# Kernel tuning notes

Hardware: AMD Instinct MI355X
Metric: run time of the kernel (lower is better)

The kernel has to match this reference:

```python
import jax, jax.numpy as jnp
import numpy as np


def force_fn(x):
    # Harmonic force F = -grad U, U(x) = 0.5 * ||x||^2 (Ornstein-Uhlenbeck).
    return -x


def setup_inputs() -> dict:
    key = jax.random.key(0)
    x0 = jax.random.normal(key, (100000, 3), dtype=jnp.float32)
    return {
        "x0": x0,
        "gamma": jnp.ones((1,), dtype=jnp.float32),
        "kT": jnp.ones((1,), dtype=jnp.float32),
        "dt": jnp.ones((1,), dtype=jnp.float32) * 0.01,
        "n_steps": 1000,
        "store_every": 10,
    }


def reference(x0, gamma, kT, dt, n_steps, store_every):
    # Overdamped Langevin: x_{t+1} = x_t + F(x_t)/gamma * dt + sqrt(2*kT*dt/gamma) * N(0, I)
    gamma_s = gamma.reshape(())
    kT_s = kT.reshape(())
    dt_s = dt.reshape(())
    noise_scale = jnp.sqrt(2.0 * kT_s * dt_s / gamma_s)

    n_chunks = n_steps // store_every  # trajectory stored every `store_every` steps
    keys = jax.random.split(jax.random.key(42), n_chunks * store_every)
    keys = keys.reshape((n_chunks, store_every))

    def step(x, k):
        noise = jax.random.normal(k, x.shape, x.dtype)
        x_new = x + force_fn(x) / gamma_s * dt_s + noise_scale * noise
        return x_new, None

    def chunk(x, ks):
        x, _ = jax.lax.scan(step, x, ks)
        return x, x  # carry and store the state after each chunk

    _, traj = jax.lax.scan(chunk, x0, keys)  # (n_chunks, N, 3)
    return jnp.concatenate([x0[None], traj], axis=0)  # (n_chunks + 1, N, 3)
```

## Files before the change

### kernel.cpp

```cpp
#include <hip/hip_runtime.h>


#define KCAP 1024

__device__ __forceinline__ unsigned rotl(unsigned v, int r) {
    return __builtin_rotateleft32(v, r);
}

__device__ __forceinline__ void tf2x32(unsigned k0, unsigned k1,
                                       unsigned x0, unsigned x1,
                                       unsigned &o0, unsigned &o1) {
    const unsigned ks2 = k0 ^ k1 ^ 0x1BD11BDAu;
    x0 += k0; x1 += k1;
#define RND(r) { x0 += x1; x1 = rotl(x1, r); x1 ^= x0; }
    RND(13) RND(15) RND(26) RND(6)
    x0 += k1;  x1 += ks2 + 1u;
    RND(17) RND(29) RND(16) RND(24)
    x0 += ks2; x1 += k0 + 2u;
    RND(13) RND(15) RND(26) RND(6)
    x0 += k0;  x1 += k1 + 3u;
    RND(17) RND(29) RND(16) RND(24)
    x0 += k1;  x1 += ks2 + 4u;
    RND(13) RND(15) RND(26) RND(6)
    x0 += ks2; x1 += k0 + 5u;
#undef RND
    o0 = x0; o1 = x1;
}

__device__ __forceinline__ float poly_lo(float w) {
    float p =        2.81022636e-08f;
    p = fmaf(p, w,   3.43273939e-07f);
    p = fmaf(p, w,  -3.5233877e-06f);
    p = fmaf(p, w,  -4.39150654e-06f);
    p = fmaf(p, w,   0.00021858087f);
    p = fmaf(p, w,  -0.00125372503f);
    p = fmaf(p, w,  -0.00417768164f);
    p = fmaf(p, w,   0.246640727f);
    p = fmaf(p, w,   1.50140941f);
    return p;
}
__device__ __forceinline__ float poly_hi(float s) {
    float p =       -0.000200214257f;
    p = fmaf(p, s,   0.000100950558f);
    p = fmaf(p, s,   0.00134934322f);
    p = fmaf(p, s,  -0.00367342844f);
    p = fmaf(p, s,   0.00573950773f);
    p = fmaf(p, s,  -0.0076224613f);
    p = fmaf(p, s,   0.00943887047f);
    p = fmaf(p, s,   1.00167406f);
    p = fmaf(p, s,   2.83297682f);
    return p;
}

__device__ __forceinline__ float lang_step(float x, uint4 k, unsigned t,
                                           float scale2, float na) {
    unsigned x1 = k.y + t;
    unsigned x0 = k.w + t;
    x1 = rotl(x1, 13) ^ x0;
#define RND(r) { x0 += x1; x1 = rotl(x1, r); x1 ^= x0; }
    RND(15) RND(26) RND(6)
    x0 += k.y; x1 += k.z + 1u;
    RND(17) RND(29) RND(16) RND(24)
    x0 += k.z; x1 += k.x + 2u;
    RND(13) RND(15) RND(26) RND(6)
    x0 += k.x; x1 += k.y + 3u;
    RND(17) RND(29) RND(16) RND(24)
    x0 += k.y; x1 += k.z + 4u;
    RND(13) RND(15) RND(26) RND(6)
    x0 += k.z; x1 += k.x + 5u;
#undef RND
    unsigned bits = x0 ^ x1;

    unsigned fb = (bits >> 9) | 0x3f800000u;
    float F = __uint_as_float(fb);
    float u = fmaf(F, 2.0f, -3.0f);
    u = fmaxf(u, -0.99999994f);
    float h = fmaf(-u, u, 1.0f);
#if __has_builtin(__builtin_amdgcn_logf)
    float l2 = __builtin_amdgcn_logf(h);
#else
    float l2 = __log2f(h);
#endif
    float p;
    if (__builtin_expect(__any(l2 <= -7.2134752f), 0)) {
        float w  = l2 * -0.69314718f;
        float p1 = poly_lo(w - 2.5f);
        float p2 = poly_hi(sqrtf(w) - 3.0f);
        p = (l2 > -7.2134752f) ? p1 : p2;
    } else {
        p = poly_lo(fmaf(l2, -0.69314718f, -2.5f));
    }
    return fmaf(scale2, p * u, fmaf(na, x, x));
}

__global__ __launch_bounds__(256) void expand_keys(uint4* __restrict__ kw) {
    unsigned j = blockIdx.x * 256 + threadIdx.x;
    if (j < KCAP) {
        unsigned b0, b1;
        tf2x32(0u, 42u, 0u, j, b0, b1);
        kw[j] = make_uint4(b0, b1, b0 ^ b1 ^ 0x1BD11BDAu, b0 + b1);
    }
}

template <bool GK>
__global__ __launch_bounds__(256) void OverdampedLangevin_62362925138458_kernel(
    const float* __restrict__ x0p,
    const float* __restrict__ gamma_p,
    const float* __restrict__ kT_p,
    const float* __restrict__ dt_p,
    const int*   __restrict__ nsteps_p,
    const int*   __restrict__ store_p,
    const uint4* __restrict__ kw,
    float*       __restrict__ out,
    int E)
{
    extern __shared__ uint4 ksh[];
    const int n_steps = *nsteps_p;
    const int store_every = *store_p;

    if (!GK) {
        const int nk = n_steps < KCAP ? n_steps : KCAP;
        for (int j = threadIdx.x; j < nk; j += blockDim.x) {
            unsigned b0, b1;
            tf2x32(0u, 42u, 0u, (unsigned)j, b0, b1);
            ksh[j] = make_uint4(b0, b1, b0 ^ b1 ^ 0x1BD11BDAu, b0 + b1);
        }
        __syncthreads();
    }

    const unsigned t = blockIdx.x * blockDim.x + threadIdx.x;
    if ((int)t >= E) return;

    const float g  = gamma_p[0];
    const float kT = kT_p[0];
    const float dt = dt_p[0];
    const float scale2 = sqrtf(2.0f * kT * dt / g) * 1.41421356f;
    const float na = -(dt / g);

    float x = x0p[t];
    out[t] = x;

    if (store_every == 10 && n_steps % 10 == 0 && n_steps <= KCAP) {
        const int nc = n_steps / 10;
        float* op = out + (size_t)E + t;
        int idx = 0;
        for (int c = 0; c < nc; ++c) {
#pragma unroll
            for (int s = 0; s < 10; ++s) {
                const uint4 k = GK ? kw[idx + s] : ksh[idx + s];
                x = lang_step(x, k, t, scale2, na);
            }
            idx += 10;
            *op = x;
            op += (size_t)E;
        }
    } else {
        int frame = 1, since = 0;
#pragma unroll 1
        for (int s = 0; s < n_steps; ++s) {
            uint4 k;
            if (s < KCAP) k = GK ? kw[s] : ksh[s];
            else {
                unsigned b0, b1;
                tf2x32(0u, 42u, 0u, (unsigned)s, b0, b1);
                k = make_uint4(b0, b1, b0 ^ b1 ^ 0x1BD11BDAu, b0 + b1);
            }
            x = lang_step(x, k, t, scale2, na);
            if (++since == store_every) {
                since = 0;
                out[(size_t)frame * (size_t)E + t] = x;
                ++frame;
            }
        }
    }
}

extern "C" void kernel_launch(void* const* d_in, const int* in_sizes, int n_in,
                              void* d_out, int out_size, void* d_ws, size_t ws_size,
                              hipStream_t stream) {
    const float* x0    = (const float*)d_in[0];
    const float* gam   = (const float*)d_in[1];
    const float* kT    = (const float*)d_in[2];
    const float* dt    = (const float*)d_in[3];
    const int*   nst   = (const int*)d_in[4];
    const int*   sev   = (const int*)d_in[5];
    float*       out   = (float*)d_out;

    const int E = in_sizes[0];
    const int blocks = (E + 255) / 256;

    if (ws_size >= KCAP * sizeof(uint4)) {
        uint4* kw = (uint4*)d_ws;
        expand_keys<<<(KCAP + 255) / 256, 256, 0, stream>>>(kw);
        OverdampedLangevin_62362925138458_kernel<true><<<blocks, 256, 0, stream>>>(
            x0, gam, kT, dt, nst, sev, kw, out, E);
    } else {
        OverdampedLangevin_62362925138458_kernel<false>
            <<<blocks, 256, KCAP * sizeof(uint4), stream>>>(
            x0, gam, kT, dt, nst, sev, nullptr, out, E);
    }
}
```

Baseline: 723.3 us.

## Precompute threefry subkeys at compile time into constant memory table

Builds the 1024 per-step threefry subkeys with a constexpr generator and places them in __constant__ memory. This removes the separate key-expansion kernel launch and the global or shared key loads. The inner chunk now computes ten normals independently before the serial x update, which exposes ILP, and an alignbit intrinsic builds the float mantissa. The keys are a fixed function of the seed in the reference, so this is legitimate, but it uses more registers for the z[10] buffer.

```diff
diff --git a/kernel.cpp b/kernel.cpp
--- a/kernel.cpp
+++ b/kernel.cpp
@@ -2,29 +2,39 @@
 
 
 #define KCAP 1024
+
+struct alignas(16) Rec { unsigned s, b, c, a; };
+struct KTable { Rec r[KCAP]; };
+
+constexpr unsigned crotl(unsigned v, int r) { return (v << r) | (v >> (32 - r)); }
+
+constexpr KTable gen_keys() {
+    KTable t{};
+    for (unsigned j = 0; j < KCAP; ++j) {
+        const unsigned k0 = 0u, k1 = 42u, ks2 = k0 ^ k1 ^ 0x1BD11BDAu;
+        unsigned x0 = 0u + k0, x1 = j + k1;
+        const int rots[20] = {13,15,26,6, 17,29,16,24, 13,15,26,6, 17,29,16,24, 13,15,26,6};
+        int ri = 0;
+        for (int blk = 0; blk < 5; ++blk) {
+            for (int rr = 0; rr < 4; ++rr) { x0 += x1; x1 = crotl(x1, rots[ri++]); x1 ^= x0; }
+            switch (blk) {
+                case 0: x0 += k1;  x1 += ks2 + 1u; break;
+                case 1: x0 += ks2; x1 += k0 + 2u;  break;
+                case 2: x0 += k0;  x1 += k1 + 3u;  break;
+                case 3: x0 += k1;  x1 += ks2 + 4u; break;
+                case 4: x0 += ks2; x1 += k0 + 5u;  break;
+            }
+        }
+        const unsigned b0 = x0, b1 = x1;
+        t.r[j] = Rec{b0 + b1, b1, b0 ^ b1 ^ 0x1BD11BDAu, b0};
+    }
+    return t;
+}
+
+__constant__ KTable KTAB = gen_keys();
 
 __device__ __forceinline__ unsigned rotl(unsigned v, int r) {
     return __builtin_rotateleft32(v, r);
-}
-
-__device__ __forceinline__ void tf2x32(unsigned k0, unsigned k1,
-                                       unsigned x0, unsigned x1,
-                                       unsigned &o0, unsigned &o1) {
-    const unsigned ks2 = k0 ^ k1 ^ 0x1BD11BDAu;
-    x0 += k0; x1 += k1;
-#define RND(r) { x0 += x1; x1 = rotl(x1, r); x1 ^= x0; }
-    RND(13) RND(15) RND(26) RND(6)
-    x0 += k1;  x1 += ks2 + 1u;
-    RND(17) RND(29) RND(16) RND(24)
-    x0 += ks2; x1 += k0 + 2u;
-    RND(13) RND(15) RND(26) RND(6)
-    x0 += k0;  x1 += k1 + 3u;
-    RND(17) RND(29) RND(16) RND(24)
-    x0 += k1;  x1 += ks2 + 4u;
-    RND(13) RND(15) RND(26) RND(6)
-    x0 += ks2; x1 += k0 + 5u;
-#undef RND
-    o0 = x0; o1 = x1;
 }
 
 __device__ __forceinline__ float poly_lo(float w) {
@@ -52,26 +62,29 @@
     return p;
 }
 
-__device__ __forceinline__ float lang_step(float x, uint4 k, unsigned t,
-                                           float scale2, float na) {
-    unsigned x1 = k.y + t;
-    unsigned x0 = k.w + t;
+__device__ __forceinline__ float normal_of(Rec k, unsigned t) {
+    unsigned x1 = k.b + t;
+    unsigned x0 = k.s + t;
     x1 = rotl(x1, 13) ^ x0;
 #define RND(r) { x0 += x1; x1 = rotl(x1, r); x1 ^= x0; }
     RND(15) RND(26) RND(6)
-    x0 += k.y; x1 += k.z + 1u;
-    RND(17) RND(29) RND(16) RND(24)
-    x0 += k.z; x1 += k.x + 2u;
-    RND(13) RND(15) RND(26) RND(6)
-    x0 += k.x; x1 += k.y + 3u;
-    RND(17) RND(29) RND(16) RND(24)
-    x0 += k.y; x1 += k.z + 4u;
-    RND(13) RND(15) RND(26) RND(6)
-    x0 += k.z; x1 += k.x + 5u;
+    x0 += k.b; x1 += k.c + 1u;
+    RND(17) RND(29) RND(16) RND(24)
+    x0 += k.c; x1 += k.a + 2u;
+    RND(13) RND(15) RND(26) RND(6)
+    x0 += k.a; x1 += k.b + 3u;
+    RND(17) RND(29) RND(16) RND(24)
+    x0 += k.b; x1 += k.c + 4u;
+    RND(13) RND(15) RND(26) RND(6)
+    x0 += k.c; x1 += k.a + 5u;
 #undef RND
     unsigned bits = x0 ^ x1;
 
+#if __has_builtin(__builtin_amdgcn_alignbit)
+    unsigned fb = __builtin_amdgcn_alignbit(0x7Fu, bits, 9u);
+#else
     unsigned fb = (bits >> 9) | 0x3f800000u;
+#endif
     float F = __uint_as_float(fb);
     float u = fmaf(F, 2.0f, -3.0f);
     u = fmaxf(u, -0.99999994f);
@@ -90,19 +103,28 @@
     } else {
         p = poly_lo(fmaf(l2, -0.69314718f, -2.5f));
     }
-    return fmaf(scale2, p * u, fmaf(na, x, x));
-}
-
-__global__ __launch_bounds__(256) void expand_keys(uint4* __restrict__ kw) {
-    unsigned j = blockIdx.x * 256 + threadIdx.x;
-    if (j < KCAP) {
-        unsigned b0, b1;
-        tf2x32(0u, 42u, 0u, j, b0, b1);
-        kw[j] = make_uint4(b0, b1, b0 ^ b1 ^ 0x1BD11BDAu, b0 + b1);
-    }
-}
-
-template <bool GK>
+    return p * u;
+}
+
+__device__ __forceinline__ Rec make_key(unsigned j) {
+    const unsigned k0 = 0u, k1 = 42u, ks2 = k0 ^ k1 ^ 0x1BD11BDAu;
+    unsigned x0 = k0, x1 = j + k1;
+#define RND(r) { x0 += x1; x1 = rotl(x1, r); x1 ^= x0; }
+    RND(13) RND(15) RND(26) RND(6)
+    x0 += k1;  x1 += ks2 + 1u;
+    RND(17) RND(29) RND(16) RND(24)
+    x0 += ks2; x1 += k0 + 2u;
+    RND(13) RND(15) RND(26) RND(6)
+    x0 += k0;  x1 += k1 + 3u;
+    RND(17) RND(29) RND(16) RND(24)
+    x0 += k1;  x1 += ks2 + 4u;
+    RND(13) RND(15) RND(26) RND(6)
+    x0 += ks2; x1 += k0 + 5u;
+#undef RND
+    Rec r; r.s = x0 + x1; r.b = x1; r.c = x0 ^ x1 ^ 0x1BD11BDAu; r.a = x0;
+    return r;
+}
+
 __global__ __launch_bounds__(256) void OverdampedLangevin_62362925138458_kernel(
     const float* __restrict__ x0p,
     const float* __restrict__ gamma_p,
@@ -110,23 +132,11 @@
     const float* __restrict__ dt_p,
     const int*   __restrict__ nsteps_p,
     const int*   __restrict__ store_p,
-    const uint4* __restrict__ kw,
     float*       __restrict__ out,
     int E)
 {
-    extern __shared__ uint4 ksh[];
     const int n_steps = *nsteps_p;
     const int store_every = *store_p;
-
-    if (!GK) {
-        const int nk = n_steps < KCAP ? n_steps : KCAP;
-        for (int j = threadIdx.x; j < nk; j += blockDim.x) {
-            unsigned b0, b1;
-            tf2x32(0u, 42u, 0u, (unsigned)j, b0, b1);
-            ksh[j] = make_uint4(b0, b1, b0 ^ b1 ^ 0x1BD11BDAu, b0 + b1);
-        }
-        __syncthreads();
-    }
 
     const unsigned t = blockIdx.x * blockDim.x + threadIdx.x;
     if ((int)t >= E) return;
@@ -145,11 +155,13 @@
         float* op = out + (size_t)E + t;
         int idx = 0;
         for (int c = 0; c < nc; ++c) {
+            float z[10];
 #pragma unroll
-            for (int s = 0; s < 10; ++s) {
-                const uint4 k = GK ? kw[idx + s] : ksh[idx + s];
-                x = lang_step(x, k, t, scale2, na);
-            }
+            for (int s = 0; s < 10; ++s)
+                z[s] = normal_of(KTAB.r[idx + s], t);
+#pragma unroll
+            for (int s = 0; s < 10; ++s)
+                x = fmaf(scale2, z[s], fmaf(na, x, x));
             idx += 10;
             *op = x;
             op += (size_t)E;
@@ -158,14 +170,9 @@
         int frame = 1, since = 0;
 #pragma unroll 1
         for (int s = 0; s < n_steps; ++s) {
-            uint4 k;
-            if (s < KCAP) k = GK ? kw[s] : ksh[s];
-            else {
-                unsigned b0, b1;
-                tf2x32(0u, 42u, 0u, (unsigned)s, b0, b1);
-                k = make_uint4(b0, b1, b0 ^ b1 ^ 0x1BD11BDAu, b0 + b1);
-            }
-            x = lang_step(x, k, t, scale2, na);
+            Rec k = (s < KCAP) ? KTAB.r[s] : make_key((unsigned)s);
+            float zz = normal_of(k, t);
+            x = fmaf(scale2, zz, fmaf(na, x, x));
             if (++since == store_every) {
                 since = 0;
                 out[(size_t)frame * (size_t)E + t] = x;
@@ -188,15 +195,6 @@
 
     const int E = in_sizes[0];
     const int blocks = (E + 255) / 256;
-
-    if (ws_size >= KCAP * sizeof(uint4)) {
-        uint4* kw = (uint4*)d_ws;
-        expand_keys<<<(KCAP + 255) / 256, 256, 0, stream>>>(kw);
-        OverdampedLangevin_62362925138458_kernel<true><<<blocks, 256, 0, stream>>>(
-            x0, gam, kT, dt, nst, sev, kw, out, E);
-    } else {
-        OverdampedLangevin_62362925138458_kernel<false>
-            <<<blocks, 256, KCAP * sizeof(uint4), stream>>>(
-            x0, gam, kT, dt, nst, sev, nullptr, out, E);
-    }
-}
+    OverdampedLangevin_62362925138458_kernel<<<blocks, 256, 0, stream>>>(
+        x0, gam, kT, dt, nst, sev, out, E);
+}
```

Result: no change. 716.2 us (-1.0%).
